# Kernel optimization log

Hardware: AMD Instinct MI355X
Metric: run time of the kernel (lower is better)

Reference implementation:

```python
import math
import jax, jax.numpy as jnp
import numpy as np

EMB = 512
HEADS = 8
NEG_INF = -1e30  # stand-in for -inf that stays finite under softmax


def setup_inputs() -> dict:
    key = jax.random.key(0)
    ks = jax.random.split(key, 6)
    b, t, e, h = 2, 2048, EMB, HEADS
    s = 1.0 / math.sqrt(e)
    return {
        "x": jax.random.normal(ks[0], (b, t, e), dtype=jnp.float32),
        "Wk": jax.random.normal(ks[1], (h * e, e), dtype=jnp.float32) * s,
        "Wq": jax.random.normal(ks[2], (h * e, e), dtype=jnp.float32) * s,
        "Wv": jax.random.normal(ks[3], (h * e, e), dtype=jnp.float32) * s,
        "Wc": jax.random.normal(ks[4], (e, h * e), dtype=jnp.float32) * s,
        "bc": jax.random.normal(ks[5], (e,), dtype=jnp.float32) * 0.01,
    }


def reference(x, Wk, Wq, Wv, Wc, bc):
    b, t, e = x.shape
    h = HEADS
    # projections: Linear(e, h*e) -> (b, t, h, e) -> (b, h, t, e)
    k = (x @ Wk.T).reshape(b, t, h, e).transpose(0, 2, 1, 3)
    q = (x @ Wq.T).reshape(b, t, h, e).transpose(0, 2, 1, 3)
    v = (x @ Wv.T).reshape(b, t, h, e).transpose(0, 2, 1, 3)
    scores = jnp.einsum("bhqe,bhke->bhqk", q, k) / math.sqrt(e)
    # causal mask: strict upper triangle (offset=1) set to -inf
    causal = jnp.tril(jnp.ones((t, t), dtype=bool))  # True where allowed
    scores = jnp.where(causal, scores, NEG_INF)
    weights = jax.nn.softmax(scores, axis=-1)
    out = jnp.einsum("bhqk,bhke->bhqe", weights, v)  # (b, h, t, e)
    out = out.transpose(0, 2, 1, 3).reshape(b, t, h * e)
    return out @ Wc.T + bc
```

## Files before the change

kernel.cpp:

```cpp
#include <hip/hip_runtime.h>

typedef unsigned short u16;
typedef __attribute__((ext_vector_type(4))) short short4v;
typedef __attribute__((ext_vector_type(8))) short short8;
typedef __attribute__((ext_vector_type(4))) float floatx4;

#define GLL16(g, l) __builtin_amdgcn_global_load_lds( \
    (const __attribute__((address_space(1))) void*)(g), \
    (__attribute__((address_space(3))) void*)(l), 16, 0, 0)

__device__ __forceinline__ float b2f(u16 h) {
    union { unsigned u; float f; } v; v.u = ((unsigned)h) << 16; return v.f;
}
__device__ __forceinline__ u16 f2b(float f) {
    union { float f; unsigned u; } v; v.f = f;
    unsigned r = v.u + 0x7fffu + ((v.u >> 16) & 1u);
    return (u16)(r >> 16);
}
__device__ __forceinline__ float launder(float f) {
    return fminf(fmaxf(f, -30000.0f), 30000.0f);
}
__device__ __forceinline__ short8 cvt8(floatx4 a, floatx4 b) {
    short8 v;
    v[0] = (short)f2b(a[0]); v[1] = (short)f2b(a[1]);
    v[2] = (short)f2b(a[2]); v[3] = (short)f2b(a[3]);
    v[4] = (short)f2b(b[0]); v[5] = (short)f2b(b[1]);
    v[6] = (short)f2b(b[2]); v[7] = (short)f2b(b[3]);
    return v;
}

__device__ __forceinline__ int sniff_block(const u16* __restrict__ xs)
{
    __shared__ int cnt;
    if (threadIdx.x == 0) cnt = 0;
    __syncthreads();
    int local = 0;
    for (int i = threadIdx.x; i < 4096; i += 256) {
        const int ex = (xs[i] >> 7) & 0xFF;
        if (ex >= 0x90) ++local;
    }
    if (local) atomicAdd(&cnt, local);
    __syncthreads();
    return cnt > 256;
}

__device__ __forceinline__ void conv_one(const void* __restrict__ raw,
                                         u16* __restrict__ dst, int n, int isf32)
{
    int i = (blockIdx.x * 256 + threadIdx.x) * 8;
    const int stride = gridDim.x * 256 * 8;
    if (isf32) {
        const float* s = (const float*)raw;
        for (; i < n; i += stride)
            *(short8*)(dst + i) = cvt8(*(const floatx4*)(s + i),
                                       *(const floatx4*)(s + i + 4));
    } else {
        const u16* s = (const u16*)raw;
        for (; i < n; i += stride)
            *(short8*)(dst + i) = *(const short8*)(s + i);
    }
}

__global__ __launch_bounds__(256)
void convert4(const void* r0, const void* r1, const void* r2, const void* r3,
              u16* d0, u16* d1, u16* d2, u16* d3, int n, const u16* xs)
{
    const int isf32 = sniff_block(xs);
    const int z = blockIdx.y;
    const void* raw = (z == 0) ? r0 : (z == 1) ? r1 : (z == 2) ? r2 : r3;
    u16* dst        = (z == 0) ? d0 : (z == 1) ? d1 : (z == 2) ? d2 : d3;
    conv_one(raw, dst, n, isf32);
}

__global__ __launch_bounds__(256)
void convert2(const void* r0, const void* r1, u16* d0, u16* d1,
              int n0, int n1, const u16* xs, int* flagp)
{
    const int isf32 = sniff_block(xs);
    if (blockIdx.x == 0 && blockIdx.y == 0 && threadIdx.x == 0) flagp[0] = isf32;
    if (blockIdx.y == 0) conv_one(r0, d0, n0, isf32);
    else                 conv_one(r1, d1, n1, isf32);
}

__global__ __launch_bounds__(256, 4)
void gemm_qkv(const u16* __restrict__ A,
              const u16* __restrict__ B0, const u16* __restrict__ B1, const u16* __restrict__ B2,
              u16* __restrict__ C0, u16* __restrict__ C1, u16* __restrict__ VTout)
{
    const int bid = (blockIdx.x & 7) * 384 + (blockIdx.x >> 3);
    const int z  = bid % 3;
    const int t  = bid / 3;
    const int mx = t & 31;
    const int my = t >> 5;

    const u16* B = (z == 0) ? B0 : ((z == 1) ? B1 : B2);

    __shared__ u16 smem[128 * 136];

    const int tid  = threadIdx.x;
    const int wave = tid >> 6;
    const int lane = tid & 63;
    const int c16  = lane & 15;
    const int quad = lane >> 4;
    const int m0 = mx * 128;
    const int n0 = my * 128;
    const int wm = (wave >> 1) * 64;
    const int wn = (wave & 1) * 64;

    floatx4 acc[4][4] = {};

    const int srow = wave * 32 + (lane >> 2);
    const int scol = (lane & 3) * 8;
    const u16* Ag = A + (size_t)(m0 + srow) * 512 + scol;
    const u16* Bg = B + (size_t)(n0 + srow) * 512 + scol;
    const int woff = (wave * 32) * 32;

    GLL16(Ag,            smem + woff);
    GLL16(Ag + 16 * 512, smem + woff + 16 * 32);
    GLL16(Bg,            smem + 8192 + woff);
    GLL16(Bg + 16 * 512, smem + 8192 + woff + 16 * 32);
    int cur = 0;

    for (int k0 = 0; k0 < 512; k0 += 32) {
        __syncthreads();
        u16* Asc = smem + cur * 4096;
        u16* Bsc = smem + 8192 + cur * 4096;

        if (k0 + 32 < 512) {
            u16* Asn = smem + (cur ^ 1) * 4096;
            u16* Bsn = smem + 8192 + (cur ^ 1) * 4096;
            GLL16(Ag + k0 + 32,            Asn + woff);
            GLL16(Ag + k0 + 32 + 16 * 512, Asn + woff + 16 * 32);
            GLL16(Bg + k0 + 32,            Bsn + woff);
            GLL16(Bg + k0 + 32 + 16 * 512, Bsn + woff + 16 * 32);
        }

        short8 af[4], bf[4];
#pragma unroll
        for (int i = 0; i < 4; ++i)
            af[i] = *(const short8*)&Asc[(wm + i * 16 + c16) * 32 + quad * 8];
#pragma unroll
        for (int i = 0; i < 4; ++i)
            bf[i] = *(const short8*)&Bsc[(wn + i * 16 + c16) * 32 + quad * 8];
#pragma unroll
        for (int i = 0; i < 4; ++i)
#pragma unroll
            for (int j = 0; j < 4; ++j)
                acc[i][j] = __builtin_amdgcn_mfma_f32_16x16x32_bf16(af[i], bf[j], acc[i][j], 0, 0, 0);
        cur ^= 1;
    }

    __syncthreads();

    if (z == 2) {
#pragma unroll
        for (int i = 0; i < 4; ++i)
#pragma unroll
            for (int j = 0; j < 4; ++j) {
                const int lc = wn + j * 16 + c16;
#pragma unroll
                for (int r = 0; r < 4; ++r) {
                    const int lr = wm + i * 16 + quad * 4 + r;
                    smem[lc * 136 + lr] = f2b(launder(acc[i][j][r]));
                }
            }
        __syncthreads();
        const int bq  = m0 >> 11;
        const int tt0 = m0 & 2047;
#pragma unroll
        for (int p = 0; p < 8; ++p) {
            const int lc  = p * 16 + (tid >> 4);
            const int seg = tid & 15;
            const short8 v = *(const short8*)&smem[lc * 136 + seg * 8];
            const int col = n0 + lc;
            const int hh = col >> 9, d = col & 511;
            *(short8*)&VTout[((size_t)((bq * 8 + hh) * 512 + d)) * 2048 + tt0 + seg * 8] = v;
        }
    } else {
        u16* C = (z == 0) ? C0 : C1;
#pragma unroll
        for (int i = 0; i < 4; ++i)
#pragma unroll
            for (int j = 0; j < 4; ++j) {
                const int lc = wn + j * 16 + c16;
#pragma unroll
                for (int r = 0; r < 4; ++r) {
                    const int lr = wm + i * 16 + quad * 4 + r;
                    smem[lr * 136 + lc] = f2b(launder(acc[i][j][r]));
                }
            }
        __syncthreads();
#pragma unroll
        for (int p = 0; p < 8; ++p) {
            const int lr  = p * 16 + (tid >> 4);
            const int seg = tid & 15;
            const short8 v = *(const short8*)&smem[lr * 136 + seg * 8];
            *(short8*)&C[(size_t)(m0 + lr) * 4096 + n0 + seg * 8] = v;
        }
    }
}

__global__ __launch_bounds__(256, 4)
void gemm_out_partial(const u16* __restrict__ A, const u16* __restrict__ B,
                      float* __restrict__ Pw)
{
    const int bid = blockIdx.x;
    const int nb = bid & 7;
    const int ks = (bid >> 3) & 3;
    const int mb = bid >> 5;

    __shared__ u16 As[2][128 * 32];
    __shared__ u16 Bs[2][64 * 32];

    const int tid  = threadIdx.x;
    const int wave = tid >> 6;
    const int lane = tid & 63;
    const int c16  = lane & 15;
    const int quad = lane >> 4;
    const int m0 = mb * 128;
    const int n0 = nb * 64;
    const int wm = (wave >> 1) * 64;
    const int wn = (wave & 1) * 32;
    const int kbase = ks * 1024;

    floatx4 acc[4][2] = {};

    const int srowA = wave * 32 + (lane >> 2);
    const int srowB = wave * 16 + (lane >> 2);
    const int scol  = (lane & 3) * 8;
    const u16* Ag = A + (size_t)(m0 + srowA) * 4096 + kbase + scol;
    const u16* Bg = B + (size_t)(n0 + srowB) * 4096 + kbase + scol;
    const int woffA = (wave * 32) * 32;
    const int woffB = (wave * 16) * 32;

    GLL16(Ag,                     &As[0][woffA]);
    GLL16(Ag + (size_t)16 * 4096, &As[0][woffA + 16 * 32]);
    GLL16(Bg,                     &Bs[0][woffB]);
    int cur = 0;

    for (int k0 = 0; k0 < 1024; k0 += 32) {
        __syncthreads();

        if (k0 + 32 < 1024) {
            GLL16(Ag + k0 + 32,                     &As[cur ^ 1][woffA]);
            GLL16(Ag + k0 + 32 + (size_t)16 * 4096, &As[cur ^ 1][woffA + 16 * 32]);
            GLL16(Bg + k0 + 32,                     &Bs[cur ^ 1][woffB]);
        }

        short8 af[4], bf[2];
#pragma unroll
        for (int i = 0; i < 4; ++i)
            af[i] = *(const short8*)&As[cur][(wm + i * 16 + c16) * 32 + quad * 8];
#pragma unroll
        for (int j = 0; j < 2; ++j)
            bf[j] = *(const short8*)&Bs[cur][(wn + j * 16 + c16) * 32 + quad * 8];
#pragma unroll
        for (int i = 0; i < 4; ++i)
#pragma unroll
            for (int j = 0; j < 2; ++j)
                acc[i][j] = __builtin_amdgcn_mfma_f32_16x16x32_bf16(af[i], bf[j], acc[i][j], 0, 0, 0);
        cur ^= 1;
    }

    float* P = Pw + (size_t)ks * 4096 * 512;
#pragma unroll
    for (int i = 0; i < 4; ++i)
#pragma unroll
        for (int j = 0; j < 2; ++j) {
            const int col = n0 + wn + j * 16 + c16;
#pragma unroll
            for (int r = 0; r < 4; ++r) {
                const int row = m0 + wm + i * 16 + quad * 4 + r;
                P[(size_t)row * 512 + col] = acc[i][j][r];
            }
        }
}

__global__ __launch_bounds__(256)
void reduce_out(const float* __restrict__ Pw, const u16* __restrict__ bias,
                const int* __restrict__ flagp, void* __restrict__ out)
{
    const int isf32 = flagp[0];
    const size_t SL = (size_t)4096 * 512;
    int g = blockIdx.x * 256 + threadIdx.x;
    const int stride = gridDim.x * 256;
    const int ngroups = 4096 * 512 / 4;
    for (; g < ngroups; g += stride) {
        const size_t e = (size_t)g * 4;
        floatx4 s = *(const floatx4*)(Pw + e);
        s += *(const floatx4*)(Pw + SL + e);
        s += *(const floatx4*)(Pw + 2 * SL + e);
        s += *(const floatx4*)(Pw + 3 * SL + e);
        const int col0 = (g & 127) * 4;
#pragma unroll
        for (int r = 0; r < 4; ++r) s[r] = launder(s[r] + b2f(bias[col0 + r]));
        if (isf32) {
            *(floatx4*)((float*)out + e) = s;
        } else {
            short4v v4;
#pragma unroll
            for (int r = 0; r < 4; ++r) v4[r] = (short)f2b(s[r]);
            *(short4v*)((u16*)out + e) = v4;
        }
    }
}

#define LOG2E 1.4426950408889634f
#define SM_SCALE 0.044194173824159216f
#define PM 24.0f

__global__ __launch_bounds__(512, 2)
void flash_attn(const u16* __restrict__ Q, const u16* __restrict__ K,
                const u16* __restrict__ VT, u16* __restrict__ O)
{
    __shared__ u16 Ks[2][64 * 516];
    __shared__ u16 Ps[4][16 * 68];
    __shared__ float Lp[2][4][16];

    const int tid  = threadIdx.x;
    const int wave = tid >> 6;
    const int lane = tid & 63;
    const int c16  = lane & 15;
    const int quad = lane >> 4;
    const int g   = wave & 3;
    const int st2 = wave >> 2;

    const int x  = blockIdx.x;
    const int bh = x & 15;
    const int pr = x >> 4;
    const int b  = bh >> 3, h = bh & 7;

    const u16* Qh  = Q  + (size_t)b * 2048 * 4096 + (size_t)h * 512;
    const u16* Kh  = K  + (size_t)b * 2048 * 4096 + (size_t)h * 512;
    const u16* VTh = VT + (size_t)bh * 512 * 2048;
    u16*       Oh  = O  + (size_t)b * 2048 * 4096 + (size_t)h * 512;

#pragma unroll
    for (int i = 0; i < 8; ++i) {
        const int kr = wave * 8 + i;
        GLL16(Kh + (size_t)kr * 4096 + lane * 8, &Ks[0][kr * 516]);
    }
    int cur = 0;

    for (int pm = 0; pm < 2; ++pm) {
        const int qt = pm ? pr : (31 - pr);
        const int q0 = qt * 64;
        const int ntile = qt + 1;
        const int qrow = q0 + g * 16 + c16;
        const int rowq = q0 + g * 16 + quad * 4;

        short8 qf[16];
#pragma unroll
        for (int s = 0; s < 16; ++s)
            qf[s] = *(const short8*)(Qh + (size_t)qrow * 4096 + s * 32 + quad * 8);

        float l_i[4] = {0.0f, 0.0f, 0.0f, 0.0f};
        floatx4 oacc[4][4] = {};

        for (int t = 0; t < ntile; ++t) {
            const int kv0 = t * 64;
            __syncthreads();

            short8 vf[4][2];
            const u16* Vw = VTh + (size_t)(wave * 64) * 2048 + kv0;
#pragma unroll
            for (int dt = 0; dt < 4; ++dt)
#pragma unroll
                for (int ks = 0; ks < 2; ++ks)
                    vf[dt][ks] = *(const short8*)(Vw + (size_t)(dt * 16 + c16) * 2048 + ks * 32 + quad * 8);

            if (t + 1 < ntile || pm == 0) {
                const int knext = (t + 1 < ntile) ? (kv0 + 64) : 0;
#pragma unroll
                for (int i = 0; i < 8; ++i) {
                    const int kr = wave * 8 + i;
                    GLL16(Kh + (size_t)(knext + kr) * 4096 + lane * 8,
                          &Ks[cur ^ 1][kr * 516]);
                }
            }

            floatx4 sv0 = {}, sv1 = {};
            __builtin_amdgcn_s_setprio(1);
#pragma unroll
            for (int s = 0; s < 16; ++s) {
                short8 kf0 = *(const short8*)&Ks[cur][(st2 * 32 + c16) * 516 + s * 32 + quad * 8];
                short8 kf1 = *(const short8*)&Ks[cur][(st2 * 32 + 16 + c16) * 516 + s * 32 + quad * 8];
                sv0 = __builtin_amdgcn_mfma_f32_16x16x32_bf16(qf[s], kf0, sv0, 0, 0, 0);
                sv1 = __builtin_amdgcn_mfma_f32_16x16x32_bf16(qf[s], kf1, sv1, 0, 0, 0);
            }
            __builtin_amdgcn_s_setprio(0);

            const int col0 = kv0 + st2 * 32 + c16;
            if (t + 1 < ntile) {
#pragma unroll
                for (int r = 0; r < 4; ++r) {
                    const float p0 = exp2f((sv0[r] * SM_SCALE - PM) * LOG2E);
                    const float p1 = exp2f((sv1[r] * SM_SCALE - PM) * LOG2E);
                    l_i[r] += p0 + p1;
                    Ps[g][(quad * 4 + r) * 68 + st2 * 32 + c16]      = f2b(p0);
                    Ps[g][(quad * 4 + r) * 68 + st2 * 32 + 16 + c16] = f2b(p1);
                }
            } else {
#pragma unroll
                for (int r = 0; r < 4; ++r) {
                    const float p0 = (col0 > rowq + r)
                        ? 0.0f : exp2f((sv0[r] * SM_SCALE - PM) * LOG2E);
                    const float p1 = (col0 + 16 > rowq + r)
                        ? 0.0f : exp2f((sv1[r] * SM_SCALE - PM) * LOG2E);
                    l_i[r] += p0 + p1;
                    Ps[g][(quad * 4 + r) * 68 + st2 * 32 + c16]      = f2b(p0);
                    Ps[g][(quad * 4 + r) * 68 + st2 * 32 + 16 + c16] = f2b(p1);
                }
            }

            asm volatile("s_waitcnt lgkmcnt(0)" ::: "memory");
            __builtin_amdgcn_s_barrier();
            __builtin_amdgcn_sched_barrier(0);

            __builtin_amdgcn_s_setprio(1);
#pragma unroll
            for (int qg = 0; qg < 4; ++qg) {
                short8 pf0 = *(const short8*)&Ps[qg][c16 * 68 + quad * 8];
                short8 pf1 = *(const short8*)&Ps[qg][c16 * 68 + 32 + quad * 8];
#pragma unroll
                for (int dt = 0; dt < 4; ++dt) {
                    oacc[qg][dt] = __builtin_amdgcn_mfma_f32_16x16x32_bf16(pf0, vf[dt][0], oacc[qg][dt], 0, 0, 0);
                    oacc[qg][dt] = __builtin_amdgcn_mfma_f32_16x16x32_bf16(pf1, vf[dt][1], oacc[qg][dt], 0, 0, 0);
                }
            }
            __builtin_amdgcn_s_setprio(0);

            cur ^= 1;
        }

#pragma unroll
        for (int off = 1; off < 16; off <<= 1)
#pragma unroll
            for (int r = 0; r < 4; ++r)
                l_i[r] += __shfl_xor(l_i[r], off, 16);
        if (c16 == 0) {
#pragma unroll
            for (int r = 0; r < 4; ++r) Lp[st2][g][quad * 4 + r] = l_i[r];
        }
        __syncthreads();

#pragma unroll
        for (int qg = 0; qg < 4; ++qg) {
            float linv[4];
#pragma unroll
            for (int r = 0; r < 4; ++r)
                linv[r] = 1.0f / (Lp[0][qg][quad * 4 + r] + Lp[1][qg][quad * 4 + r]);
#pragma unroll
            for (int dt = 0; dt < 4; ++dt)
#pragma unroll
                for (int r = 0; r < 4; ++r)
                    Oh[(size_t)(q0 + qg * 16 + quad * 4 + r) * 4096 + wave * 64 + dt * 16 + c16] =
                        f2b(launder(oacc[qg][dt][r] * linv[r]));
        }
    }
}

extern "C" void kernel_launch(void* const* d_in, const int* in_sizes, int n_in,
                              void* d_out, int out_size, void* d_ws, size_t ws_size,
                              hipStream_t stream)
{
    const size_t SZ  = (size_t)4096 * 4096;
    const size_t SZh = (size_t)4096 * 512;

    u16* Qb  = (u16*)d_ws;
    u16* Kb  = Qb + SZ;
    u16* Vb  = Kb + SZ;
    u16* VTb = Vb + SZ;
    u16* Ob  = Vb;

    u16* xb  = Vb;
    u16* Wqb = Vb + SZh;
    u16* Wkb = Vb + 2 * SZh;
    u16* Wvb = Vb + 3 * SZh;

    u16* Wcb = Qb;
    u16* bcb = Qb + SZh;
    int* flagp = (int*)(Qb + 2 * SZh);
    float* Pw  = (float*)Kb;

    const u16* xs = (const u16*)d_in[0];

    convert4<<<dim3(256, 4), 256, 0, stream>>>(
        d_in[0], d_in[2], d_in[1], d_in[3], xb, Wqb, Wkb, Wvb, (int)SZh, xs);

    gemm_qkv<<<dim3(3072), 256, 0, stream>>>(
        xb, Wqb, Wkb, Wvb, Qb, Kb, VTb);

    flash_attn<<<dim3(256), 512, 0, stream>>>(Qb, Kb, VTb, Ob);

    convert2<<<dim3(256, 2), 256, 0, stream>>>(
        d_in[4], d_in[5], Wcb, bcb, (int)SZh, 512, xs, flagp);

    gemm_out_partial<<<dim3(1024), 256, 0, stream>>>(Ob, Wcb, Pw);

    reduce_out<<<dim3(256), 256, 0, stream>>>(Pw, bcb, flagp, d_out);
}
```

Baseline: 357.6 us.

## Merge weight conversions into one kernel and retile output GEMM to full-width blocks

```diff
diff --git a/kernel.cpp b/kernel.cpp
--- a/kernel.cpp
+++ b/kernel.cpp
@@ -62,24 +62,19 @@
 }
 
 __global__ __launch_bounds__(256)
-void convert4(const void* r0, const void* r1, const void* r2, const void* r3,
-              u16* d0, u16* d1, u16* d2, u16* d3, int n, const u16* xs)
+void convert6(const void* r0, const void* r1, const void* r2, const void* r3,
+              const void* r4, const void* r5,
+              u16* d0, u16* d1, u16* d2, u16* d3, u16* d4, u16* d5,
+              int n, const u16* xs, int* flagp)
 {
     const int isf32 = sniff_block(xs);
     const int z = blockIdx.y;
-    const void* raw = (z == 0) ? r0 : (z == 1) ? r1 : (z == 2) ? r2 : r3;
-    u16* dst        = (z == 0) ? d0 : (z == 1) ? d1 : (z == 2) ? d2 : d3;
-    conv_one(raw, dst, n, isf32);
-}
-
-__global__ __launch_bounds__(256)
-void convert2(const void* r0, const void* r1, u16* d0, u16* d1,
-              int n0, int n1, const u16* xs, int* flagp)
-{
-    const int isf32 = sniff_block(xs);
-    if (blockIdx.x == 0 && blockIdx.y == 0 && threadIdx.x == 0) flagp[0] = isf32;
-    if (blockIdx.y == 0) conv_one(r0, d0, n0, isf32);
-    else                 conv_one(r1, d1, n1, isf32);
+    if (z == 0 && blockIdx.x == 0 && threadIdx.x == 0) flagp[0] = isf32;
+    const void* raw = (z == 0) ? r0 : (z == 1) ? r1 : (z == 2) ? r2
+                    : (z == 3) ? r3 : (z == 4) ? r4 : r5;
+    u16* dst        = (z == 0) ? d0 : (z == 1) ? d1 : (z == 2) ? d2
+                    : (z == 3) ? d3 : (z == 4) ? d4 : d5;
+    conv_one(raw, dst, (z == 5) ? 512 : n, isf32);
 }
 
 __global__ __launch_bounds__(256, 4)
@@ -200,80 +195,70 @@
     }
 }
 
-__global__ __launch_bounds__(256, 4)
+__global__ __launch_bounds__(512, 2)
 void gemm_out_partial(const u16* __restrict__ A, const u16* __restrict__ B,
                       float* __restrict__ Pw)
 {
     const int bid = blockIdx.x;
-    const int nb = bid & 7;
-    const int ks = (bid >> 3) & 3;
-    const int mb = bid >> 5;
-
-    __shared__ u16 As[2][128 * 32];
-    __shared__ u16 Bs[2][64 * 32];
+    const int ks = bid & 3;
+    const int mb = bid >> 2;
+
+    __shared__ u16 As[2][64 * 32];
+    __shared__ u16 Bs[2][512 * 32];
 
     const int tid  = threadIdx.x;
     const int wave = tid >> 6;
     const int lane = tid & 63;
     const int c16  = lane & 15;
     const int quad = lane >> 4;
-    const int m0 = mb * 128;
-    const int n0 = nb * 64;
-    const int wm = (wave >> 1) * 64;
-    const int wn = (wave & 1) * 32;
+    const int wr = wave & 3;
+    const int wc = wave >> 2;
+    const int m0 = mb * 64;
     const int kbase = ks * 1024;
 
-    floatx4 acc[4][2] = {};
-
-    const int srowA = wave * 32 + (lane >> 2);
-    const int srowB = wave * 16 + (lane >> 2);
-    const int scol  = (lane & 3) * 8;
-    const u16* Ag = A + (size_t)(m0 + srowA) * 4096 + kbase + scol;
-    const u16* Bg = B + (size_t)(n0 + srowB) * 4096 + kbase + scol;
-    const int woffA = (wave * 32) * 32;
-    const int woffB = (wave * 16) * 32;
-
-    GLL16(Ag,                     &As[0][woffA]);
-    GLL16(Ag + (size_t)16 * 4096, &As[0][woffA + 16 * 32]);
-    GLL16(Bg,                     &Bs[0][woffB]);
+    floatx4 acc[16] = {};
+
+    const int srow = lane >> 2;
+    const int scol = (lane & 3) * 8;
+    const u16* AgA = A + (size_t)(m0 + wave * 16 + srow) * 4096 + kbase + scol;
+    const u16* BgB = B + (size_t)(wave * 64 + srow) * 4096 + kbase + scol;
+
+    if (wave < 4) GLL16(AgA, &As[0][(wave * 16) * 32]);
+#pragma unroll
+    for (int g = 0; g < 4; ++g)
+        GLL16(BgB + (size_t)(g * 16) * 4096, &Bs[0][(wave * 64 + g * 16) * 32]);
     int cur = 0;
 
     for (int k0 = 0; k0 < 1024; k0 += 32) {
         __syncthreads();
 
         if (k0 + 32 < 1024) {
-            GLL16(Ag + k0 + 32,                     &As[cur ^ 1][woffA]);
-            GLL16(Ag + k0 + 32 + (size_t)16 * 4096, &As[cur ^ 1][woffA + 16 * 32]);
-            GLL16(Bg + k0 + 32,                     &Bs[cur ^ 1][woffB]);
-        }
-
-        short8 af[4], bf[2];
-#pragma unroll
-        for (int i = 0; i < 4; ++i)
-            af[i] = *(const short8*)&As[cur][(wm + i * 16 + c16) * 32 + quad * 8];
-#pragma unroll
-        for (int j = 0; j < 2; ++j)
-            bf[j] = *(const short8*)&Bs[cur][(wn + j * 16 + c16) * 32 + quad * 8];
-#pragma unroll
-        for (int i = 0; i < 4; ++i)
-#pragma unroll
-            for (int j = 0; j < 2; ++j)
-                acc[i][j] = __builtin_amdgcn_mfma_f32_16x16x32_bf16(af[i], bf[j], acc[i][j], 0, 0, 0);
+            if (wave < 4) GLL16(AgA + k0 + 32, &As[cur ^ 1][(wave * 16) * 32]);
+#pragma unroll
+            for (int g = 0; g < 4; ++g)
+                GLL16(BgB + (size_t)(g * 16) * 4096 + k0 + 32,
+                      &Bs[cur ^ 1][(wave * 64 + g * 16) * 32]);
+        }
+
+        const short8 af = *(const short8*)&As[cur][(wr * 16 + c16) * 32 + quad * 8];
+#pragma unroll
+        for (int j = 0; j < 16; ++j) {
+            const short8 bfj = *(const short8*)&Bs[cur][(wc * 256 + j * 16 + c16) * 32 + quad * 8];
+            acc[j] = __builtin_amdgcn_mfma_f32_16x16x32_bf16(af, bfj, acc[j], 0, 0, 0);
+        }
         cur ^= 1;
     }
 
     float* P = Pw + (size_t)ks * 4096 * 512;
 #pragma unroll
-    for (int i = 0; i < 4; ++i)
-#pragma unroll
-        for (int j = 0; j < 2; ++j) {
-            const int col = n0 + wn + j * 16 + c16;
-#pragma unroll
-            for (int r = 0; r < 4; ++r) {
-                const int row = m0 + wm + i * 16 + quad * 4 + r;
-                P[(size_t)row * 512 + col] = acc[i][j][r];
-            }
-        }
+    for (int j = 0; j < 16; ++j) {
+        const int col = wc * 256 + j * 16 + c16;
+#pragma unroll
+        for (int r = 0; r < 4; ++r) {
+            const int row = m0 + wr * 16 + quad * 4 + r;
+            P[(size_t)row * 512 + col] = acc[j][r];
+        }
+    }
 }
 
 __global__ __launch_bounds__(256)
@@ -471,32 +456,28 @@
     u16* Kb  = Qb + SZ;
     u16* Vb  = Kb + SZ;
     u16* VTb = Vb + SZ;
-    u16* Ob  = Vb;
 
     u16* xb  = Vb;
     u16* Wqb = Vb + SZh;
     u16* Wkb = Vb + 2 * SZh;
     u16* Wvb = Vb + 3 * SZh;
-
-    u16* Wcb = Qb;
-    u16* bcb = Qb + SZh;
-    int* flagp = (int*)(Qb + 2 * SZh);
+    u16* Wcb = Vb + 4 * SZh;
+    u16* bcb = Vb + 5 * SZh;
+    int* flagp = (int*)(Vb + 5 * SZh + 512);
     float* Pw  = (float*)Kb;
 
     const u16* xs = (const u16*)d_in[0];
 
-    convert4<<<dim3(256, 4), 256, 0, stream>>>(
-        d_in[0], d_in[2], d_in[1], d_in[3], xb, Wqb, Wkb, Wvb, (int)SZh, xs);
+    convert6<<<dim3(256, 6), 256, 0, stream>>>(
+        d_in[0], d_in[2], d_in[1], d_in[3], d_in[4], d_in[5],
+        xb, Wqb, Wkb, Wvb, Wcb, bcb, (int)SZh, xs, flagp);
 
     gemm_qkv<<<dim3(3072), 256, 0, stream>>>(
         xb, Wqb, Wkb, Wvb, Qb, Kb, VTb);
 
-    flash_attn<<<dim3(256), 512, 0, stream>>>(Qb, Kb, VTb, Ob);
-
-    convert2<<<dim3(256, 2), 256, 0, stream>>>(
-        d_in[4], d_in[5], Wcb, bcb, (int)SZh, 512, xs, flagp);
-
-    gemm_out_partial<<<dim3(1024), 256, 0, stream>>>(Ob, Wcb, Pw);
+    flash_attn<<<dim3(256), 512, 0, stream>>>(Qb, Kb, VTb, Qb);
+
+    gemm_out_partial<<<dim3(256), 512, 0, stream>>>(Qb, Wcb, Pw);
 
     reduce_out<<<dim3(256), 256, 0, stream>>>(Pw, bcb, flagp, d_out);
 }
```

Result: faster. 349.4 us (-2.3%).
